# Kernel optimization log

Hardware: AMD Instinct MI355X
Metric: run time of the kernel (lower is better)

## Reference

```python
import jax, jax.numpy as jnp
import numpy as np

N_USER = 100000
N_ITEM = 50000
N = N_USER + N_ITEM
EMB = 64
FEAT = 384
NNZ = 2400000
N_PROMPT = 8
N_LAYERS = 4
EPS = 1e-8


def setup_inputs() -> dict:
    key = jax.random.key(0)
    ks = jax.random.split(key, 8)
    user_fea = jax.random.normal(ks[0], (N_USER, EMB), jnp.float32)
    item_fea = jax.random.normal(ks[1], (N_ITEM, FEAT), jnp.float32)
    prompt_embedding = jax.random.normal(ks[2], (N_PROMPT, EMB), jnp.float32)
    mlp_w = jax.random.normal(ks[3], (FEAT, EMB), jnp.float32) / np.sqrt(FEAT)
    mlp_b = jnp.zeros((EMB,), jnp.float32)
    adj_rows = jax.random.randint(ks[4], (NNZ,), 0, N, jnp.int32)
    adj_cols = jax.random.randint(ks[5], (NNZ,), 0, N, jnp.int32)
    # normalized-adjacency-like positive values
    adj_vals = jax.random.uniform(ks[6], (NNZ,), jnp.float32) * 0.01
    return dict(user_fea=user_fea, item_fea=item_fea,
                prompt_embedding=prompt_embedding, mlp_w=mlp_w, mlp_b=mlp_b,
                adj_rows=adj_rows, adj_cols=adj_cols, adj_vals=adj_vals)


def _spmm(rows, cols, vals, x):
    # sparse [N,N] @ dense [N,E] via gather + segment-sum
    return jax.ops.segment_sum(vals[:, None] * x[cols], rows, num_segments=N)


def reference(user_fea, item_fea, prompt_embedding, mlp_w, mlp_b,
              adj_rows, adj_cols, adj_vals):
    prompt_embd = jnp.sum(prompt_embedding, axis=0)            # [EMB]
    user_embd = user_fea + prompt_embd[None, :]                # [N_USER, EMB]
    item_embd = jnp.tanh(item_fea @ mlp_w + mlp_b)             # [N_ITEM, EMB]
    ego = jnp.concatenate([user_embd, item_embd], axis=0)      # [N, EMB]
    ego_norm = jnp.linalg.norm(ego, axis=-1)                   # [N]

    x = ego
    acc = ego  # running sum over layer stack (layer 0 = ego)
    for _ in range(N_LAYERS):
        x = _spmm(adj_rows, adj_cols, adj_vals, x)
        # cosine similarity of propagated embedding vs ego embedding, per row
        denom = jnp.maximum(jnp.linalg.norm(x, axis=-1) * ego_norm, EPS)
        w = jnp.sum(x * ego, axis=-1) / denom                  # [N]
        x = w[:, None] * x
        acc = acc + x

    return acc[:N_USER], acc[N_USER:]
```

## Files before the change

kernel.cpp:

```cpp
#include <hip/hip_runtime.h>
#include <hip/hip_fp16.h>

constexpr int kNUser = 100000;
constexpr int kNItem = 50000;
constexpr int kN     = 150000;
constexpr int kEmb   = 64;
constexpr int kFeat  = 384;
constexpr int kNnz   = 2400000;
constexpr float kEps = 1e-8f;

constexpr int kNBkt   = 256;
constexpr int kBR     = (kN + kNBkt - 1) / kNBkt;
constexpr int kChunkA = 4096;
constexpr int kNWGA   = (kNnz + kChunkA - 1) / kChunkA;

constexpr int kKS     = kFeat / 32;
constexpr int kNT     = kEmb / 16;
constexpr int kWElems = kKS * kNT * 64 * 8;

typedef __attribute__((ext_vector_type(8))) short short8v;
typedef __attribute__((ext_vector_type(4))) float floatx4;

__device__ inline unsigned short f2bf(float f) {
    unsigned u = __float_as_uint(f);
    return (unsigned short)((u + 0x7FFFu + ((u >> 16) & 1u)) >> 16);
}
__device__ inline float bf2f(unsigned short h) {
    return __uint_as_float((unsigned)h << 16);
}


__global__ void prompt_sum_k(const float* __restrict__ p, float* __restrict__ out) {
    int d = threadIdx.x;
    float s = 0.f;
#pragma unroll
    for (int i = 0; i < 8; ++i) s += p[i * kEmb + d];
    out[d] = s;
}

__global__ void user_ego_k(const float* __restrict__ uf, const float* __restrict__ ps,
                           float* __restrict__ ego) {
    int i = blockIdx.x * blockDim.x + threadIdx.x;
    if (i >= kNUser * kEmb) return;
    ego[i] = uf[i] + ps[i & 63];
}

__global__ void wsplit_k(const float* __restrict__ w, unsigned short* __restrict__ whi,
                         unsigned short* __restrict__ wlo) {
    int t = blockIdx.x * 256 + threadIdx.x;
    if (t >= kWElems) return;
    int j    = t & 7;
    int lane = (t >> 3) & 63;
    int nt   = (t >> 9) & 3;
    int ks   = t >> 11;
    int k = ks * 32 + (lane >> 4) * 8 + j;
    int n = nt * 16 + (lane & 15);
    float v = w[k * kEmb + n];
    unsigned short h = f2bf(v);
    whi[t] = h;
    wlo[t] = f2bf(v - bf2f(h));
}

__global__ __launch_bounds__(256)
void item_ego_mfma_k(const float* __restrict__ itf, const unsigned short* __restrict__ whi,
                     const unsigned short* __restrict__ wlo, const float* __restrict__ b,
                     float* __restrict__ ego) {
    int t    = threadIdx.x;
    int wid  = t >> 6;
    int lane = t & 63;
    int r0   = blockIdx.x * 64 + wid * 16;
    int arow = r0 + (lane & 15);
    int kg   = lane >> 4;
    bool av  = arow < kNItem;
    const float* ap = itf + (size_t)(av ? arow : 0) * kFeat + kg * 8;

    const short8v* whv = (const short8v*)whi;
    const short8v* wlv = (const short8v*)wlo;

    floatx4 accH[kNT], accL[kNT];
#pragma unroll
    for (int nt = 0; nt < kNT; ++nt) {
        accH[nt] = (floatx4){0.f, 0.f, 0.f, 0.f};
        accL[nt] = (floatx4){0.f, 0.f, 0.f, 0.f};
    }

    for (int ks = 0; ks < kKS; ++ks) {
        const float4 z = make_float4(0.f, 0.f, 0.f, 0.f);
        float4 a0 = av ? *(const float4*)(ap + ks * 32)     : z;
        float4 a1 = av ? *(const float4*)(ap + ks * 32 + 4) : z;
        short8v ah, al;
#pragma unroll
        for (int j = 0; j < 8; ++j) {
            float f = (j < 4) ? ((const float*)&a0)[j] : ((const float*)&a1)[j - 4];
            unsigned short h = f2bf(f);
            ah[j] = (short)h;
            al[j] = (short)f2bf(f - bf2f(h));
        }
#pragma unroll
        for (int nt = 0; nt < kNT; ++nt) {
            short8v bh = whv[(ks * kNT + nt) * 64 + lane];
            short8v bl = wlv[(ks * kNT + nt) * 64 + lane];
            accH[nt] = __builtin_amdgcn_mfma_f32_16x16x32_bf16(ah, bh, accH[nt], 0, 0, 0);
            accL[nt] = __builtin_amdgcn_mfma_f32_16x16x32_bf16(ah, bl, accL[nt], 0, 0, 0);
            accL[nt] = __builtin_amdgcn_mfma_f32_16x16x32_bf16(al, bh, accL[nt], 0, 0, 0);
        }
    }

    int col0  = lane & 15;
    int rsub  = (lane >> 4) * 4;
#pragma unroll
    for (int nt = 0; nt < kNT; ++nt) {
        float bb = b[nt * 16 + col0];
#pragma unroll
        for (int r = 0; r < 4; ++r) {
            int row = r0 + rsub + r;
            if (row < kNItem)
                ego[(size_t)(kNUser + row) * kEmb + nt * 16 + col0] =
                    tanhf(accH[nt][r] + accL[nt][r] + bb);
        }
    }
}

constexpr int kRW      = 16;
constexpr int kRowsBlk = 64;
constexpr int kKc      = 32;

__global__ __launch_bounds__(256, 2)
void item_ego_k(const float* __restrict__ itf, const float* __restrict__ w,
                const float* __restrict__ b, float* __restrict__ ego) {
    __shared__ float lds_a[kRowsBlk * kKc];
    int t      = threadIdx.x;
    int wid    = t >> 6;
    int lane   = t & 63;
    int blk_r0 = blockIdx.x * kRowsBlk;

    float acc[kRW];
#pragma unroll
    for (int r = 0; r < kRW; ++r) acc[r] = 0.f;

    int srow = t >> 3;
    int scol = (t & 7) * 4;

    for (int kc = 0; kc < kFeat; kc += kKc) {
        __syncthreads();
        {
            const float4 z = make_float4(0.f, 0.f, 0.f, 0.f);
            int gr0 = blk_r0 + srow;
            int gr1 = gr0 + 32;
            float4 v0 = (gr0 < kNItem)
                ? *(const float4*)(itf + (size_t)gr0 * kFeat + kc + scol) : z;
            float4 v1 = (gr1 < kNItem)
                ? *(const float4*)(itf + (size_t)gr1 * kFeat + kc + scol) : z;
            *(float4*)(lds_a + srow * kKc + scol)        = v0;
            *(float4*)(lds_a + (srow + 32) * kKc + scol) = v1;
        }
        float wreg[kKc];
#pragma unroll
        for (int k = 0; k < kKc; ++k) wreg[k] = w[(kc + k) * kEmb + lane];
        __syncthreads();
#pragma unroll
        for (int r = 0; r < kRW; ++r) {
            const float4* av = (const float4*)(lds_a + (wid * kRW + r) * kKc);
#pragma unroll
            for (int q = 0; q < 8; ++q) {
                float4 a = av[q];
                acc[r] = fmaf(a.x, wreg[q * 4 + 0], acc[r]);
                acc[r] = fmaf(a.y, wreg[q * 4 + 1], acc[r]);
                acc[r] = fmaf(a.z, wreg[q * 4 + 2], acc[r]);
                acc[r] = fmaf(a.w, wreg[q * 4 + 3], acc[r]);
            }
        }
    }
    float bv = b[lane];
#pragma unroll
    for (int r = 0; r < kRW; ++r) {
        int row = blk_r0 + wid * kRW + r;
        if (row < kNItem)
            ego[(size_t)(kNUser + row) * kEmb + lane] = tanhf(acc[r] + bv);
    }
}

__global__ void norm_init_csr_k(const float* __restrict__ ego, float* __restrict__ nrm,
                                unsigned short* __restrict__ egoh) {
    int wid  = threadIdx.x >> 6;
    int lane = threadIdx.x & 63;
    int row  = blockIdx.x * 4 + wid;
    if (row >= kN) return;
    size_t idx = (size_t)row * kEmb + lane;
    float e = ego[idx];
    __half h = __float2half_rn(e);
    egoh[idx] = *(unsigned short*)&h;
    float s = e * e;
#pragma unroll
    for (int o = 32; o >= 1; o >>= 1) s += __shfl_xor(s, o, 64);
    if (lane == 0) nrm[row] = sqrtf(s);
}


__global__ __launch_bounds__(256)
void bcnt_k(const int* __restrict__ rows, int* __restrict__ bcnt) {
    __shared__ int cnt[kNBkt];
    int t  = threadIdx.x;
    int e0 = blockIdx.x * kChunkA;
    for (int i = t; i < kNBkt; i += 256) cnt[i] = 0;
    __syncthreads();
#pragma unroll
    for (int k = 0; k < kChunkA / 256; ++k) {
        int e = e0 + k * 256 + t;
        if (e < kNnz) atomicAdd(&cnt[rows[e] / kBR], 1);
    }
    __syncthreads();
    for (int i = t; i < kNBkt; i += 256)
        if (cnt[i]) atomicAdd(&bcnt[i], cnt[i]);
}

__global__ void bscan_k(const int* __restrict__ bcnt, int* __restrict__ bbase,
                        int* __restrict__ bfill) {
    __shared__ int sd[kNBkt];
    int t = threadIdx.x;
    int v = bcnt[t];
    sd[t] = v;
    __syncthreads();
#pragma unroll
    for (int off = 1; off < kNBkt; off <<= 1) {
        int u = (t >= off) ? sd[t - off] : 0;
        __syncthreads();
        sd[t] += u;
        __syncthreads();
    }
    bbase[t] = sd[t] - v;
    if (t == kNBkt - 1) bbase[kNBkt] = kNnz;
    bfill[t] = 0;
}

__global__ __launch_bounds__(256)
void bucket_k(const int* __restrict__ rows, const int* __restrict__ cols,
              const float* __restrict__ vals, const int* __restrict__ bbase,
              int* __restrict__ bfill, int2* __restrict__ tmp) {
    __shared__ int cnt[kNBkt];
    __shared__ int wgbase[kNBkt];
    int t  = threadIdx.x;
    int e0 = blockIdx.x * kChunkA;
    for (int i = t; i < kNBkt; i += 256) cnt[i] = 0;
    __syncthreads();
    int myb[kChunkA / 256];
    int myoff[kChunkA / 256];
#pragma unroll
    for (int k = 0; k < kChunkA / 256; ++k) {
        int e = e0 + k * 256 + t;
        if (e < kNnz) {
            int b = rows[e] / kBR;
            myb[k]   = b;
            myoff[k] = atomicAdd(&cnt[b], 1);
        } else {
            myb[k] = -1;
        }
    }
    __syncthreads();
    for (int i = t; i < kNBkt; i += 256)
        wgbase[i] = cnt[i] ? atomicAdd(&bfill[i], cnt[i]) : 0;
    __syncthreads();
#pragma unroll
    for (int k = 0; k < kChunkA / 256; ++k) {
        int b = myb[k];
        if (b < 0) continue;
        int e = e0 + k * 256 + t;
        int pos = bbase[b] + wgbase[b] + myoff[k];
        int rowrel = rows[e] - b * kBR;
        tmp[pos] = make_int2((rowrel << 18) | cols[e], __float_as_int(vals[e]));
    }
}

__global__ __launch_bounds__(256)
void debucket2_k(const int2* __restrict__ tmp, const int* __restrict__ bbase,
                 int* __restrict__ rp, int2* __restrict__ csr) {
    __shared__ int rcnt[kBR];
    __shared__ int rbaseL[kBR];
    __shared__ int sd[256];
    int b  = blockIdx.x;
    int t  = threadIdx.x;
    int j0 = bbase[b];
    int j1 = bbase[b + 1];
    for (int i = t; i < kBR; i += 256) rcnt[i] = 0;
    __syncthreads();
    for (int j = j0 + t; j < j1; j += 256)
        atomicAdd(&rcnt[(unsigned)tmp[j].x >> 18], 1);
    __syncthreads();
    int base = t * 3;
    int c0 = (base     < kBR) ? rcnt[base]     : 0;
    int c1 = (base + 1 < kBR) ? rcnt[base + 1] : 0;
    int c2 = (base + 2 < kBR) ? rcnt[base + 2] : 0;
    int tsum = c0 + c1 + c2;
    sd[t] = tsum;
    __syncthreads();
#pragma unroll
    for (int off = 1; off < 256; off <<= 1) {
        int u = (t >= off) ? sd[t - off] : 0;
        __syncthreads();
        sd[t] += u;
        __syncthreads();
    }
    int g0 = j0 + sd[t] - tsum;
    if (base     < kBR) rbaseL[base]     = g0;
    if (base + 1 < kBR) rbaseL[base + 1] = g0 + c0;
    if (base + 2 < kBR) rbaseL[base + 2] = g0 + c0 + c1;
    __syncthreads();
    int rbaseG = b * kBR;
    for (int i = t; i < kBR; i += 256) {
        int r = rbaseG + i;
        if (r < kN) rp[r] = rbaseL[i];
    }
    if (b == kNBkt - 1 && t == 0) rp[kN] = kNnz;
    for (int i = t; i < kBR; i += 256) rcnt[i] = 0;
    __syncthreads();
    for (int j = j0 + t; j < j1; j += 256) {
        int2 e = tmp[j];
        int rr = (unsigned)e.x >> 18;
        int pos = rbaseL[rr] + atomicAdd(&rcnt[rr], 1);
        csr[pos] = make_int2(e.x & 0x3FFFF, e.y);
    }
}

__global__ __launch_bounds__(256)
void layer_k(const int* __restrict__ rp, const int2* __restrict__ csr,
             const float* __restrict__ ego, const float* __restrict__ nrm,
             const unsigned short* __restrict__ xin_h,
             unsigned short* __restrict__ xout_h,
             const unsigned short* __restrict__ xh1,
             const unsigned short* __restrict__ xh2,
             float* __restrict__ acc, int last) {
    int wid  = threadIdx.x >> 6;
    int lane = threadIdx.x & 63;
    int row  = blockIdx.x * 4 + wid;
    if (row >= kN) return;
    int q   = lane >> 4;
    int sub = lane & 15;
    int p0 = rp[row];
    int p1 = rp[row + 1];

    float4 s = make_float4(0.f, 0.f, 0.f, 0.f);
    for (int base = p0; base < p1; base += 16) {
        int2  e[4];
        float w[4];
#pragma unroll
        for (int g = 0; g < 4; ++g) {
            int j  = base + g * 4 + q;
            bool v = j < p1;
            e[g] = csr[v ? j : p0];
            w[g] = v ? __int_as_float(e[g].y) : 0.f;
        }
        uint2 gv[4];
#pragma unroll
        for (int g = 0; g < 4; ++g)
            gv[g] = *(const uint2*)(xin_h + (size_t)e[g].x * kEmb + sub * 4);
#pragma unroll
        for (int g = 0; g < 4; ++g) {
            float2 f0 = __half22float2(*(const __half2*)&gv[g].x);
            float2 f1 = __half22float2(*(const __half2*)&gv[g].y);
            s.x = fmaf(w[g], f0.x, s.x);
            s.y = fmaf(w[g], f0.y, s.y);
            s.z = fmaf(w[g], f1.x, s.z);
            s.w = fmaf(w[g], f1.y, s.w);
        }
    }
#pragma unroll
    for (int o = 16; o <= 32; o <<= 1) {
        s.x += __shfl_xor(s.x, o, 64);
        s.y += __shfl_xor(s.y, o, 64);
        s.z += __shfl_xor(s.z, o, 64);
        s.w += __shfl_xor(s.w, o, 64);
    }
    size_t idx = (size_t)row * kEmb + sub * 4;
    const float4 ev = *(const float4*)(ego + idx);
    float d = s.x * ev.x + s.y * ev.y + s.z * ev.z + s.w * ev.w;
    float n = s.x * s.x + s.y * s.y + s.z * s.z + s.w * s.w;
#pragma unroll
    for (int o = 1; o <= 8; o <<= 1) {
        d += __shfl_xor(d, o, 64);
        n += __shfl_xor(n, o, 64);
    }
    float wgt = d / fmaxf(sqrtf(n) * nrm[row], kEps);
    if (q == 0) {
        float4 xw = make_float4(wgt * s.x, wgt * s.y, wgt * s.z, wgt * s.w);
        if (!last) {
            __half2 o0 = __floats2half2_rn(xw.x, xw.y);
            __half2 o1 = __floats2half2_rn(xw.z, xw.w);
            uint2 st;
            st.x = *(unsigned*)&o0;
            st.y = *(unsigned*)&o1;
            *(uint2*)(xout_h + idx) = st;
        } else {
            uint2 a1 = *(const uint2*)(xh1 + idx);
            uint2 a2 = *(const uint2*)(xh2 + idx);
            uint2 a3 = *(const uint2*)(xin_h + idx);
            float2 f1a = __half22float2(*(const __half2*)&a1.x);
            float2 f1b = __half22float2(*(const __half2*)&a1.y);
            float2 f2a = __half22float2(*(const __half2*)&a2.x);
            float2 f2b = __half22float2(*(const __half2*)&a2.y);
            float2 f3a = __half22float2(*(const __half2*)&a3.x);
            float2 f3b = __half22float2(*(const __half2*)&a3.y);
            float4 out;
            out.x = ev.x + f1a.x + f2a.x + f3a.x + xw.x;
            out.y = ev.y + f1a.y + f2a.y + f3a.y + xw.y;
            out.z = ev.z + f1b.x + f2b.x + f3b.x + xw.z;
            out.w = ev.w + f1b.y + f2b.y + f3b.y + xw.w;
            *(float4*)(acc + idx) = out;
        }
    }
}


__global__ void norm_init_full_k(const float* __restrict__ ego, float* __restrict__ nrm,
                                 float* __restrict__ x, float* __restrict__ acc) {
    int wid  = threadIdx.x >> 6;
    int lane = threadIdx.x & 63;
    int row  = blockIdx.x * 4 + wid;
    if (row >= kN) return;
    size_t idx = (size_t)row * kEmb + lane;
    float e = ego[idx];
    x[idx]   = e;
    acc[idx] = e;
    float s = e * e;
#pragma unroll
    for (int o = 32; o >= 1; o >>= 1) s += __shfl_xor(s, o, 64);
    if (lane == 0) nrm[row] = sqrtf(s);
}

__global__ void spmm_k(const int* __restrict__ rows, const int* __restrict__ cols,
                       const float* __restrict__ vals, const float* __restrict__ x,
                       float* __restrict__ y) {
    long long t = (long long)blockIdx.x * blockDim.x + threadIdx.x;
    int e = (int)(t >> 6);
    if (e >= kNnz) return;
    int lane = threadIdx.x & 63;
    atomicAdd(y + (size_t)rows[e] * kEmb + lane, vals[e] * x[(size_t)cols[e] * kEmb + lane]);
}

__global__ void weight_k(const float* __restrict__ ego, const float* __restrict__ nrm,
                         const float* __restrict__ y, float* __restrict__ x,
                         float* __restrict__ acc) {
    int wid  = threadIdx.x >> 6;
    int lane = threadIdx.x & 63;
    int row  = blockIdx.x * 4 + wid;
    if (row >= kN) return;
    size_t idx = (size_t)row * kEmb + lane;
    float yv = y[idx];
    float ev = ego[idx];
    float d = yv * ev;
    float n = yv * yv;
#pragma unroll
    for (int o = 32; o >= 1; o >>= 1) {
        d += __shfl_xor(d, o, 64);
        n += __shfl_xor(n, o, 64);
    }
    float w  = d / fmaxf(sqrtf(n) * nrm[row], kEps);
    float xw = w * yv;
    x[idx] = xw;
    acc[idx] += xw;
}


extern "C" void kernel_launch(void* const* d_in, const int* in_sizes, int n_in,
                              void* d_out, int out_size, void* d_ws, size_t ws_size,
                              hipStream_t stream) {
    const float* user_fea = (const float*)d_in[0];
    const float* item_fea = (const float*)d_in[1];
    const float* prompt   = (const float*)d_in[2];
    const float* mlp_w    = (const float*)d_in[3];
    const float* mlp_b    = (const float*)d_in[4];
    const int*   adj_rows = (const int*)d_in[5];
    const int*   adj_cols = (const int*)d_in[6];
    const float* adj_vals = (const float*)d_in[7];
    float* acc = (float*)d_out;

    const size_t NE = (size_t)kN * kEmb;
    float* ws = (float*)d_ws;

    size_t off = 0;
    float* f_ego = ws + off; off += NE;
    float* f_ps  = ws + off; off += 64;
    float* f_nrm = ws + off; off += kN;
    size_t branch0 = off;
    unsigned short* f_egoh = (unsigned short*)(ws + off); off += NE / 2;
    unsigned short* f_xh1  = (unsigned short*)(ws + off); off += NE / 2;
    unsigned short* f_xh2  = (unsigned short*)(ws + off); off += NE / 2;
    unsigned short* f_xh3  = (unsigned short*)(ws + off); off += NE / 2;
    int* row_ptr = (int*)(ws + off); off += kN + 1;
    int* bcnt    = (int*)(ws + off); off += kNBkt;
    int* bbase   = (int*)(ws + off); off += kNBkt + 1;
    int* bfill   = (int*)(ws + off); off += kNBkt;
    off = (off + 3) & ~(size_t)3;
    unsigned short* whi = (unsigned short*)(ws + off); off += kWElems / 2;
    unsigned short* wlo = (unsigned short*)(ws + off); off += kWElems / 2;
    off = (off + 1) & ~(size_t)1;
    int2* csr = (int2*)(ws + off); off += (size_t)kNnz * 2;
    const bool use_csr = ws_size >= off * 4;

    prompt_sum_k<<<1, 64, 0, stream>>>(prompt, f_ps);
    user_ego_k<<<(kNUser * kEmb + 255) / 256, 256, 0, stream>>>(user_fea, f_ps, f_ego);

    if (use_csr) {
        wsplit_k<<<(kWElems + 255) / 256, 256, 0, stream>>>(mlp_w, whi, wlo);
        item_ego_mfma_k<<<(kNItem + 63) / 64, 256, 0, stream>>>(item_fea, whi, wlo,
                                                                mlp_b, f_ego);

        int2* tmp = (int2*)f_xh1;
        hipMemsetAsync(bcnt, 0, kNBkt * sizeof(int), stream);
        bcnt_k<<<kNWGA, 256, 0, stream>>>(adj_rows, bcnt);
        bscan_k<<<1, kNBkt, 0, stream>>>(bcnt, bbase, bfill);
        bucket_k<<<kNWGA, 256, 0, stream>>>(adj_rows, adj_cols, adj_vals,
                                            bbase, bfill, tmp);
        debucket2_k<<<kNBkt, 256, 0, stream>>>(tmp, bbase, row_ptr, csr);

        norm_init_csr_k<<<(kN + 3) / 4, 256, 0, stream>>>(f_ego, f_nrm, f_egoh);

        layer_k<<<(kN + 3) / 4, 256, 0, stream>>>(row_ptr, csr, f_ego, f_nrm,
                                                  f_egoh, f_xh1, nullptr, nullptr,
                                                  acc, 0);
        layer_k<<<(kN + 3) / 4, 256, 0, stream>>>(row_ptr, csr, f_ego, f_nrm,
                                                  f_xh1, f_xh2, nullptr, nullptr,
                                                  acc, 0);
        layer_k<<<(kN + 3) / 4, 256, 0, stream>>>(row_ptr, csr, f_ego, f_nrm,
                                                  f_xh2, f_xh3, nullptr, nullptr,
                                                  acc, 0);
        layer_k<<<(kN + 3) / 4, 256, 0, stream>>>(row_ptr, csr, f_ego, f_nrm,
                                                  f_xh3, nullptr, f_xh1, f_xh2,
                                                  acc, 1);
    } else {
        float* f_x = ws + branch0;
        float* f_y = f_x + NE;
        item_ego_k<<<(kNItem + kRowsBlk - 1) / kRowsBlk, 256, 0, stream>>>(
            item_fea, mlp_w, mlp_b, f_ego);
        norm_init_full_k<<<(kN + 3) / 4, 256, 0, stream>>>(f_ego, f_nrm, f_x, acc);
        for (int l = 0; l < 4; ++l) {
            hipMemsetAsync(f_y, 0, NE * sizeof(float), stream);
            spmm_k<<<(int)(((long long)kNnz * 64 + 255) / 256), 256, 0, stream>>>(
                adj_rows, adj_cols, adj_vals, f_x, f_y);
            weight_k<<<(kN + 3) / 4, 256, 0, stream>>>(f_ego, f_nrm, f_y, f_x, acc);
        }
    }
}
```

Before: 711.1 us.

## Fuse ego norm and fp16 conversion into producers; drop fp32 ego buffer

The user and item ego kernels now write the fp16 ego copy and the per-row norms directly. This removes the fp32 ego buffer and the separate norm_init pass. Each layer kernel now reads the fp16 ego instead of fp32, which halves that per-layer traffic. The trade-off is lower precision in the cosine dot product and in any output that uses ego, since those values are now rounded to fp16.

```diff
diff --git a/kernel.cpp b/kernel.cpp
--- a/kernel.cpp
+++ b/kernel.cpp
@@ -43,6 +43,22 @@
     int i = blockIdx.x * blockDim.x + threadIdx.x;
     if (i >= kNUser * kEmb) return;
     ego[i] = uf[i] + ps[i & 63];
+}
+
+__global__ void user_egoh_k(const float* __restrict__ uf, const float* __restrict__ ps,
+                            unsigned short* __restrict__ egoh, float* __restrict__ nrm) {
+    int wid  = threadIdx.x >> 6;
+    int lane = threadIdx.x & 63;
+    int row  = blockIdx.x * 4 + wid;
+    if (row >= kNUser) return;
+    size_t idx = (size_t)row * kEmb + lane;
+    float e = uf[idx] + ps[lane];
+    __half h = __float2half_rn(e);
+    egoh[idx] = *(unsigned short*)&h;
+    float s = e * e;
+#pragma unroll
+    for (int o = 32; o >= 1; o >>= 1) s += __shfl_xor(s, o, 64);
+    if (lane == 0) nrm[row] = sqrtf(s);
 }
 
 __global__ void wsplit_k(const float* __restrict__ w, unsigned short* __restrict__ whi,
@@ -64,7 +80,7 @@
 __global__ __launch_bounds__(256)
 void item_ego_mfma_k(const float* __restrict__ itf, const unsigned short* __restrict__ whi,
                      const unsigned short* __restrict__ wlo, const float* __restrict__ b,
-                     float* __restrict__ ego) {
+                     unsigned short* __restrict__ egoh, float* __restrict__ nrm) {
     int t    = threadIdx.x;
     int wid  = t >> 6;
     int lane = t & 63;
@@ -106,18 +122,30 @@
         }
     }
 
-    int col0  = lane & 15;
-    int rsub  = (lane >> 4) * 4;
+    int col0 = lane & 15;
+    int rsub = (lane >> 4) * 4;
+    float sq[4] = {0.f, 0.f, 0.f, 0.f};
 #pragma unroll
     for (int nt = 0; nt < kNT; ++nt) {
         float bb = b[nt * 16 + col0];
 #pragma unroll
         for (int r = 0; r < 4; ++r) {
             int row = r0 + rsub + r;
-            if (row < kNItem)
-                ego[(size_t)(kNUser + row) * kEmb + nt * 16 + col0] =
-                    tanhf(accH[nt][r] + accL[nt][r] + bb);
-        }
+            float v = tanhf(accH[nt][r] + accL[nt][r] + bb);
+            sq[r] = fmaf(v, v, sq[r]);
+            if (row < kNItem) {
+                __half h = __float2half_rn(v);
+                egoh[(size_t)(kNUser + row) * kEmb + nt * 16 + col0] =
+                    *(unsigned short*)&h;
+            }
+        }
+    }
+#pragma unroll
+    for (int r = 0; r < 4; ++r) {
+#pragma unroll
+        for (int o = 1; o <= 8; o <<= 1) sq[r] += __shfl_xor(sq[r], o, 64);
+        int row = r0 + rsub + r;
+        if (col0 == 0 && row < kNItem) nrm[kNUser + row] = sqrtf(sq[r]);
     }
 }
 
@@ -180,22 +208,6 @@
     }
 }
 
-__global__ void norm_init_csr_k(const float* __restrict__ ego, float* __restrict__ nrm,
-                                unsigned short* __restrict__ egoh) {
-    int wid  = threadIdx.x >> 6;
-    int lane = threadIdx.x & 63;
-    int row  = blockIdx.x * 4 + wid;
-    if (row >= kN) return;
-    size_t idx = (size_t)row * kEmb + lane;
-    float e = ego[idx];
-    __half h = __float2half_rn(e);
-    egoh[idx] = *(unsigned short*)&h;
-    float s = e * e;
-#pragma unroll
-    for (int o = 32; o >= 1; o >>= 1) s += __shfl_xor(s, o, 64);
-    if (lane == 0) nrm[row] = sqrtf(s);
-}
-
 
 __global__ __launch_bounds__(256)
 void bcnt_k(const int* __restrict__ rows, int* __restrict__ bcnt) {
@@ -323,7 +335,7 @@
 
 __global__ __launch_bounds__(256)
 void layer_k(const int* __restrict__ rp, const int2* __restrict__ csr,
-             const float* __restrict__ ego, const float* __restrict__ nrm,
+             const unsigned short* __restrict__ egoh, const float* __restrict__ nrm,
              const unsigned short* __restrict__ xin_h,
              unsigned short* __restrict__ xout_h,
              const unsigned short* __restrict__ xh1,
@@ -371,7 +383,10 @@
         s.w += __shfl_xor(s.w, o, 64);
     }
     size_t idx = (size_t)row * kEmb + sub * 4;
-    const float4 ev = *(const float4*)(ego + idx);
+    uint2 evu = *(const uint2*)(egoh + idx);
+    float2 ea = __half22float2(*(const __half2*)&evu.x);
+    float2 eb = __half22float2(*(const __half2*)&evu.y);
+    float4 ev = make_float4(ea.x, ea.y, eb.x, eb.y);
     float d = s.x * ev.x + s.y * ev.y + s.z * ev.z + s.w * ev.w;
     float n = s.x * s.x + s.y * s.y + s.z * s.z + s.w * s.w;
 #pragma unroll
@@ -477,7 +492,6 @@
     float* ws = (float*)d_ws;
 
     size_t off = 0;
-    float* f_ego = ws + off; off += NE;
     float* f_ps  = ws + off; off += 64;
     float* f_nrm = ws + off; off += kN;
     size_t branch0 = off;
@@ -497,12 +511,13 @@
     const bool use_csr = ws_size >= off * 4;
 
     prompt_sum_k<<<1, 64, 0, stream>>>(prompt, f_ps);
-    user_ego_k<<<(kNUser * kEmb + 255) / 256, 256, 0, stream>>>(user_fea, f_ps, f_ego);
 
     if (use_csr) {
+        user_egoh_k<<<(kNUser + 3) / 4, 256, 0, stream>>>(user_fea, f_ps,
+                                                          f_egoh, f_nrm);
         wsplit_k<<<(kWElems + 255) / 256, 256, 0, stream>>>(mlp_w, whi, wlo);
         item_ego_mfma_k<<<(kNItem + 63) / 64, 256, 0, stream>>>(item_fea, whi, wlo,
-                                                                mlp_b, f_ego);
+                                                                mlp_b, f_egoh, f_nrm);
 
         int2* tmp = (int2*)f_xh1;
         hipMemsetAsync(bcnt, 0, kNBkt * sizeof(int), stream);
@@ -512,23 +527,24 @@
                                             bbase, bfill, tmp);
         debucket2_k<<<kNBkt, 256, 0, stream>>>(tmp, bbase, row_ptr, csr);
 
-        norm_init_csr_k<<<(kN + 3) / 4, 256, 0, stream>>>(f_ego, f_nrm, f_egoh);
-
-        layer_k<<<(kN + 3) / 4, 256, 0, stream>>>(row_ptr, csr, f_ego, f_nrm,
+        layer_k<<<(kN + 3) / 4, 256, 0, stream>>>(row_ptr, csr, f_egoh, f_nrm,
                                                   f_egoh, f_xh1, nullptr, nullptr,
                                                   acc, 0);
-        layer_k<<<(kN + 3) / 4, 256, 0, stream>>>(row_ptr, csr, f_ego, f_nrm,
+        layer_k<<<(kN + 3) / 4, 256, 0, stream>>>(row_ptr, csr, f_egoh, f_nrm,
                                                   f_xh1, f_xh2, nullptr, nullptr,
                                                   acc, 0);
-        layer_k<<<(kN + 3) / 4, 256, 0, stream>>>(row_ptr, csr, f_ego, f_nrm,
+        layer_k<<<(kN + 3) / 4, 256, 0, stream>>>(row_ptr, csr, f_egoh, f_nrm,
                                                   f_xh2, f_xh3, nullptr, nullptr,
                                                   acc, 0);
-        layer_k<<<(kN + 3) / 4, 256, 0, stream>>>(row_ptr, csr, f_ego, f_nrm,
+        layer_k<<<(kN + 3) / 4, 256, 0, stream>>>(row_ptr, csr, f_egoh, f_nrm,
                                                   f_xh3, nullptr, f_xh1, f_xh2,
                                                   acc, 1);
     } else {
-        float* f_x = ws + branch0;
-        float* f_y = f_x + NE;
+        float* f_ego = ws + branch0;
+        float* f_x   = f_ego + NE;
+        float* f_y   = f_x + NE;
+        user_ego_k<<<(kNUser * kEmb + 255) / 256, 256, 0, stream>>>(user_fea, f_ps,
+                                                                    f_ego);
         item_ego_k<<<(kNItem + kRowsBlk - 1) / kRowsBlk, 256, 0, stream>>>(
             item_fea, mlp_w, mlp_b, f_ego);
         norm_init_full_k<<<(kN + 3) / 4, 256, 0, stream>>>(f_ego, f_nrm, f_x, acc);
```

Result: faster. 687.7 us (-3.3%).
